# Kernel optimization log

Hardware: AMD Instinct MI355X
Metric: run time of the kernel (lower is better)

The kernel has to match this reference:

```python
import jax, jax.numpy as jnp
import numpy as np

NUM_EMBEDDINGS = 4096
EMBEDDING_DIM = 128
COMMITMENT_COST = 0.25


def setup_inputs() -> dict:
    key = jax.random.key(0)
    k_x, k_w = jax.random.split(key)
    inputs = jax.random.normal(k_x, (32, 128, 32, 32), dtype=jnp.float32)
    # xavier_uniform for Embedding weight [K, D]: bound = sqrt(6/(K+D))
    bound = float(np.sqrt(6.0 / (NUM_EMBEDDINGS + EMBEDDING_DIM)))
    weight = jax.random.uniform(k_w, (NUM_EMBEDDINGS, EMBEDDING_DIM),
                                dtype=jnp.float32, minval=-bound, maxval=bound)
    return {"inputs": inputs, "weight": weight}


def reference(inputs, weight):
    K, D = weight.shape
    # channels-first 4D input with C == embedding_dim -> NHWC
    x = jnp.transpose(inputs, (0, 2, 3, 1))  # [B, H, W, D]
    input_shape = x.shape
    flat = x.reshape(-1, D)                  # [N, D]

    x_sq = jnp.sum(flat * flat, axis=1, keepdims=True)          # [N, 1]
    w_sq = jnp.sum(weight * weight, axis=1)                     # [K]
    two_xy = 2.0 * jnp.matmul(flat, weight.T)                   # [N, K]
    distances = x_sq - two_xy + w_sq[None, :] + 1e-8

    encoding_indices = jnp.argmin(distances, axis=1)            # [N] int

    quantized = weight[encoding_indices].reshape(input_shape)   # [B, H, W, D]

    q_latent_loss = jnp.mean((quantized - x) ** 2)
    e_latent_loss = jnp.mean((jax.lax.stop_gradient(quantized) - x) ** 2)
    loss = q_latent_loss + COMMITMENT_COST * e_latent_loss
    loss = jnp.where(jnp.isnan(loss) | jnp.isinf(loss), jnp.float32(0.1), loss)

    quantized_st = x + jax.lax.stop_gradient(quantized - x)

    counts = jnp.zeros((K,), dtype=jnp.float32).at[encoding_indices].add(1.0)
    avg_probs = counts / encoding_indices.shape[0]
    perplexity = jnp.exp(-jnp.sum(avg_probs * jnp.log(avg_probs + 1e-10)))

    encodings = jax.nn.one_hot(encoding_indices, K, dtype=jnp.float32)  # [N, K]

    # input was channels-first -> restore NCHW
    quantized_st = jnp.transpose(quantized_st, (0, 3, 1, 2))
    return quantized_st, loss, perplexity, encodings, encoding_indices
```

## Files before the change

### kernel.cpp

```cpp
#include <hip/hip_runtime.h>
#include <stdint.h>
#include <math.h>

#define K_CODES 4096
#define DIM 128
#define N_FLAT 32768
#define HW 1024

#define OFF_Q    0
#define OFF_LOSS 4194304
#define OFF_PERP 4194305
#define OFF_ENC  4194306
#define OFF_IDX  138412034

#define WS_PACKED 0
#define WS_COUNTS 262144
#define WS_WSQ    278528
#define WS_XSQ    294912
#define WS_PART   425984
#define WS_XHL    430080
#define WS_WHL    (WS_XHL + 16777216)

typedef _Float16 f16x8 __attribute__((ext_vector_type(8)));
typedef float    f32x4 __attribute__((ext_vector_type(4)));


__global__ __launch_bounds__(256) void wsq_kernel(const float* __restrict__ w,
                                                  float* __restrict__ wsq,
                                                  float* __restrict__ counts) {
    int wave = threadIdx.x >> 6, lane = threadIdx.x & 63;
    int k = blockIdx.x * 4 + wave;
    float a = w[k * DIM + lane];
    float b = w[k * DIM + lane + 64];
    float s = a * a + b * b;
    #pragma unroll
    for (int o = 32; o > 0; o >>= 1) s += __shfl_down(s, o, 64);
    if (lane == 0) { wsq[k] = s; counts[k] = 0.f; }
}

__global__ __launch_bounds__(256) void wplanes_kernel(const float* __restrict__ w,
                                                      _Float16* __restrict__ whl) {
    int T = blockIdx.x * 256 + threadIdx.x;
    int k = T >> 2, seg = T & 3;
    const float* wp = w + (size_t)k * DIM + seg * 32;
    _Float16* row = whl + (size_t)k * 256;
    #pragma unroll
    for (int q = 0; q < 4; ++q) {
        float4 a = *(const float4*)(wp + q * 8);
        float4 b = *(const float4*)(wp + q * 8 + 4);
        float vv[8] = {a.x, a.y, a.z, a.w, b.x, b.y, b.z, b.w};
        f16x8 hv, lv;
        #pragma unroll
        for (int j = 0; j < 8; ++j) {
            float v = 1024.0f * vv[j];
            _Float16 h = (_Float16)v;
            _Float16 l = (_Float16)(v - (float)h);
            hv[j] = h; lv[j] = l;
        }
        *(f16x8*)(row + seg * 32 + q * 8) = hv;
        *(f16x8*)(row + 128 + seg * 32 + q * 8) = lv;
    }
}

__global__ __launch_bounds__(256) void xprep_kernel(const float* __restrict__ x,
                                                    _Float16* __restrict__ xhl,
                                                    float* __restrict__ xsq,
                                                    unsigned long long* __restrict__ packed) {
    __shared__ float xt[128 * 65];
    const int t = threadIdx.x;
    const int n0 = blockIdx.x * 64;
    const int b = n0 >> 10, hw0 = n0 & 1023;
    const float* xg = x + (size_t)b * (DIM * HW) + hw0;
    #pragma unroll
    for (int i = 0; i < 16; ++i) {
        int idx = i * 256 + t;
        int c = idx >> 5, n2 = (idx & 31) << 1;
        float2 v = *(const float2*)(xg + c * HW + n2);
        xt[c * 65 + n2] = v.x;
        xt[c * 65 + n2 + 1] = v.y;
    }
    __syncthreads();
    if (t < 64) {
        packed[n0 + t] = ~0ull;
        float s = 0.f;
        #pragma unroll
        for (int c = 0; c < DIM; ++c) {
            float v = xt[c * 65 + t];
            s = fmaf(v, v, s);
        }
        xsq[n0 + t] = s;
    }
    const int n = t >> 2, seg = t & 3;
    _Float16* row = xhl + (size_t)(n0 + n) * 256;
    #pragma unroll
    for (int q = 0; q < 4; ++q) {
        f16x8 hv, lv;
        #pragma unroll
        for (int j = 0; j < 8; ++j) {
            float v = 32.0f * xt[(seg * 32 + q * 8 + j) * 65 + n];
            _Float16 h = (_Float16)v;
            _Float16 l = (_Float16)(v - (float)h);
            hv[j] = h; lv[j] = l;
        }
        *(f16x8*)(row + seg * 32 + q * 8) = hv;
        *(f16x8*)(row + 128 + seg * 32 + q * 8) = lv;
    }
}

__global__ __launch_bounds__(256) void dist_argmin(
    const _Float16* __restrict__ xhl, const _Float16* __restrict__ whl,
    const float* __restrict__ wsq, const float* __restrict__ xsq,
    unsigned long long* __restrict__ packed, float* __restrict__ enc)
{
    __shared__ __align__(16) _Float16 xl[128 * 72];
    __shared__ __align__(16) _Float16 wl[128 * 72];
    __shared__ float xsq_s[128];
    __shared__ unsigned long long red[128];

    const int tid  = threadIdx.x;
    const int lane = tid & 63, wave = tid >> 6;
    const int lq   = lane & 15, quad = lane >> 4;
    const int wn0  = (wave >> 1) * 64, wk0 = (wave & 1) * 64;
    const int n0   = blockIdx.x * 128;
    const int kbase = blockIdx.y * 512;

    const int sr = tid >> 3, shh = (tid >> 2) & 1, sq = tid & 3;
    const int gbase = sr * 256 + shh * 128 + sq * 8;
    const int lbase = sr * 72  + shh * 32  + sq * 8;

    float* ebase = enc + (size_t)n0 * K_CODES + kbase;
    float* efill = ebase + (size_t)(tid >> 7) * K_CODES + 2 + (tid & 127) * 4;

    if (tid < 128) {
        float2 z2; z2.x = 0.f; z2.y = 0.f;
        *(float2*)(ebase + (size_t)tid * K_CODES) = z2;
        xsq_s[tid] = xsq[n0 + tid];
        red[tid] = ~0ull;
    }

    const _Float16* xbase = xhl + (size_t)n0 * 256;

    const _Float16* xr0 = xl + (wn0 + lq) * 72 + quad * 8;
    const _Float16* wr0 = wl + (wk0 + lq) * 72 + quad * 8;

    f16x8 px[4], pw[4];
    {
        const _Float16* wb = whl + (size_t)kbase * 256;
        #pragma unroll
        for (int i = 0; i < 4; ++i) {
            px[i] = *(const f16x8*)(xbase + gbase + i * 8192);
            pw[i] = *(const f16x8*)(wb    + gbase + i * 8192);
        }
        #pragma unroll
        for (int i = 0; i < 4; ++i) {
            *(f16x8*)(xl + lbase + i * 2304) = px[i];
            *(f16x8*)(wl + lbase + i * 2304) = pw[i];
        }
    }

    f32x4 acc[4][4];
    float wk[4];

    for (int s = 0; s < 16; ++s) {
        const int ks = s >> 2, c0 = s & 3;
        const int k0 = kbase + ks * 128;
        if (c0 == 0) {
            #pragma unroll
            for (int ki = 0; ki < 4; ++ki)
                wk[ki] = wsq[k0 + wk0 + ki * 16 + lq];
            #pragma unroll
            for (int i = 0; i < 4; ++i)
                #pragma unroll
                for (int j = 0; j < 4; ++j)
                    acc[i][j] = (f32x4){0.f, 0.f, 0.f, 0.f};
        }
        __syncthreads();

        f16x8 ah[4], al[4], bh[4], bl[4];
        #pragma unroll
        for (int i = 0; i < 4; ++i) {
            ah[i] = *(const f16x8*)(xr0 + i * 16 * 72);
            al[i] = *(const f16x8*)(xr0 + i * 16 * 72 + 32);
            bh[i] = *(const f16x8*)(wr0 + i * 16 * 72);
            bl[i] = *(const f16x8*)(wr0 + i * 16 * 72 + 32);
        }

        if (s < 15) {
            const int s1 = s + 1;
            const _Float16* wb =
                whl + (size_t)(kbase + (s1 >> 2) * 128) * 256;
            const int off = gbase + (s1 & 3) * 32;
            #pragma unroll
            for (int i = 0; i < 4; ++i) {
                px[i] = *(const f16x8*)(xbase + off + i * 8192);
                pw[i] = *(const f16x8*)(wb    + off + i * 8192);
            }
        }
        {
            float4 z4; z4.x = z4.y = z4.z = z4.w = 0.f;
            #pragma unroll
            for (int j = 0; j < 4; ++j)
                *(float4*)(efill + (size_t)(s * 8 + j * 2) * K_CODES) = z4;
        }

        #pragma unroll
        for (int ki = 0; ki < 4; ++ki)
            #pragma unroll
            for (int ni = 0; ni < 4; ++ni) {
                acc[ni][ki] = __builtin_amdgcn_mfma_f32_16x16x32_f16(
                    ah[ni], bh[ki], acc[ni][ki], 0, 0, 0);
                acc[ni][ki] = __builtin_amdgcn_mfma_f32_16x16x32_f16(
                    ah[ni], bl[ki], acc[ni][ki], 0, 0, 0);
                acc[ni][ki] = __builtin_amdgcn_mfma_f32_16x16x32_f16(
                    al[ni], bh[ki], acc[ni][ki], 0, 0, 0);
            }

        if (s < 15) {
            __syncthreads();
            #pragma unroll
            for (int i = 0; i < 4; ++i) {
                *(f16x8*)(xl + lbase + i * 2304) = px[i];
                *(f16x8*)(wl + lbase + i * 2304) = pw[i];
            }
        }

        if (c0 == 3) {
            #pragma unroll
            for (int ni = 0; ni < 4; ++ni) {
                #pragma unroll
                for (int rg = 0; rg < 4; ++rg) {
                    int rowl = wn0 + ni * 16 + quad * 4 + rg;
                    float xr = xsq_s[rowl];
                    float best = 3.4e38f; int bk = 0;
                    #pragma unroll
                    for (int ki = 0; ki < 4; ++ki) {
                        int kl = wk0 + ki * 16 + lq;
                        float t = xr - acc[ni][ki][rg] * 6.103515625e-05f;
                        t += wk[ki];
                        t += 1e-8f;
                        if (t < best) { best = t; bk = k0 + kl; }
                    }
                    unsigned u = __float_as_uint(best);
                    u = (u & 0x80000000u) ? ~u : (u | 0x80000000u);
                    unsigned long long p =
                        ((unsigned long long)u << 32) | (unsigned)bk;
                    #pragma unroll
                    for (int m = 1; m < 16; m <<= 1) {
                        unsigned long long o = __shfl_xor(p, m, 64);
                        if (o < p) p = o;
                    }
                    if (lq == 0) atomicMin(&red[rowl], p);
                }
            }
        }
    }

    __syncthreads();
    if (tid < 128) atomicMin(&packed[n0 + tid], red[tid]);
}

__global__ __launch_bounds__(256) void combine(
    const unsigned long long* __restrict__ packed,
    float* __restrict__ idxf, float* __restrict__ enc,
    float* __restrict__ counts)
{
    int n = blockIdx.x * 256 + threadIdx.x;
    unsigned k = (unsigned)(packed[n] & 0xFFFFFFFFu);
    idxf[n] = (float)k;
    enc[(size_t)n * K_CODES + k] = 1.0f;
    atomicAdd(&counts[k], 1.0f);
}

__global__ __launch_bounds__(256) void quantize_loss(
    const float* __restrict__ x, const float* __restrict__ w,
    const float* __restrict__ idxf, float* __restrict__ outq,
    float* __restrict__ part)
{
    const int base4 = (blockIdx.x * 256 + threadIdx.x) * 4;
    float s = 0.f;
    #pragma unroll
    for (int i = 0; i < 4; ++i) {
        int e  = base4 + i * 1048576;
        int hw = e & 1023;
        int c  = (e >> 10) & 127;
        int b  = e >> 17;
        int n  = (b << 10) | hw;
        float4 xv = *(const float4*)(x + e);
        float4 kf = *(const float4*)(idxf + n);
        float q0 = w[(int)kf.x * DIM + c];
        float q1 = w[(int)kf.y * DIM + c];
        float q2 = w[(int)kf.z * DIM + c];
        float q3 = w[(int)kf.w * DIM + c];
        float4 df; df.x = q0 - xv.x; df.y = q1 - xv.y;
                   df.z = q2 - xv.z; df.w = q3 - xv.w;
        float4 o;  o.x = xv.x + df.x; o.y = xv.y + df.y;
                   o.z = xv.z + df.z; o.w = xv.w + df.w;
        *(float4*)(outq + e) = o;
        s = fmaf(df.x, df.x, s);
        s = fmaf(df.y, df.y, s);
        s = fmaf(df.z, df.z, s);
        s = fmaf(df.w, df.w, s);
    }
    #pragma unroll
    for (int o = 32; o > 0; o >>= 1) s += __shfl_down(s, o, 64);
    __shared__ float ls[4];
    if ((threadIdx.x & 63) == 0) ls[threadIdx.x >> 6] = s;
    __syncthreads();
    if (threadIdx.x == 0) part[blockIdx.x] = ls[0] + ls[1] + ls[2] + ls[3];
}

__global__ __launch_bounds__(256) void finalize(
    const float* __restrict__ counts, const float* __restrict__ part,
    float* __restrict__ out)
{
    __shared__ float sh[512];
    float h = 0.f;
    for (int k = threadIdx.x; k < K_CODES; k += 256) {
        float p = counts[k] * (1.0f / N_FLAT);
        h += p * logf(p + 1e-10f);
    }
    float s = 0.f;
    for (int i = threadIdx.x; i < 1024; i += 256) s += part[i];
    sh[threadIdx.x] = h;
    sh[256 + threadIdx.x] = s;
    __syncthreads();
    #pragma unroll
    for (int st = 128; st > 0; st >>= 1) {
        if (threadIdx.x < st) {
            sh[threadIdx.x] += sh[threadIdx.x + st];
            sh[256 + threadIdx.x] += sh[256 + threadIdx.x + st];
        }
        __syncthreads();
    }
    if (threadIdx.x == 0) {
        float perp = expf(-sh[0]);
        float loss = 1.25f * (sh[256] / 4194304.0f);
        if (isnan(loss) || isinf(loss)) loss = 0.1f;
        out[OFF_LOSS] = loss;
        out[OFF_PERP] = perp;
    }
}

extern "C" void kernel_launch(void* const* d_in, const int* in_sizes, int n_in,
                              void* d_out, int out_size, void* d_ws, size_t ws_size,
                              hipStream_t stream) {
    const float* x = (const float*)d_in[0];
    const float* w = (const float*)d_in[1];
    float* out = (float*)d_out;
    char* ws = (char*)d_ws;

    unsigned long long* packed = (unsigned long long*)(ws + WS_PACKED);
    float* counts = (float*)(ws + WS_COUNTS);
    float* wsq    = (float*)(ws + WS_WSQ);
    float* xsq    = (float*)(ws + WS_XSQ);
    float* part   = (float*)(ws + WS_PART);
    _Float16* xhl = (_Float16*)(ws + WS_XHL);
    _Float16* whl = (_Float16*)(ws + WS_WHL);

    wsq_kernel<<<K_CODES / 4, 256, 0, stream>>>(w, wsq, counts);
    wplanes_kernel<<<K_CODES * 4 / 256, 256, 0, stream>>>(w, whl);
    xprep_kernel<<<N_FLAT / 64, 256, 0, stream>>>(x, xhl, xsq, packed);

    dim3 g2(256, 8);
    dist_argmin<<<g2, 256, 0, stream>>>(xhl, whl, wsq, xsq, packed,
                                        out + OFF_ENC);

    combine<<<N_FLAT / 256, 256, 0, stream>>>(packed, out + OFF_IDX,
                                              out + OFF_ENC, counts);

    quantize_loss<<<1024, 256, 0, stream>>>(x, w, out + OFF_IDX,
                                            out + OFF_Q, part);

    finalize<<<1, 256, 0, stream>>>(counts, part, out);
}
```

Baseline: 793.2 us.

## Double-buffer LDS tiles in dist_argmin and move one-hot zero-fill to memset

Tiles for x and codebook in shared memory are double-buffered, and global loads are prefetched two steps ahead, so each iteration needs only one barrier instead of two. The zeroing of the large one-hot encoding output is removed from the distance kernel and done by a separate hipMemsetAsync before the kernels. This cuts sync stalls in the MFMA loop but doubles LDS use, which may lower occupancy. It also gives up overlapping the zero-fill writes with compute.

```diff
diff --git a/kernel.cpp b/kernel.cpp
--- a/kernel.cpp
+++ b/kernel.cpp
@@ -110,10 +110,10 @@
 __global__ __launch_bounds__(256) void dist_argmin(
     const _Float16* __restrict__ xhl, const _Float16* __restrict__ whl,
     const float* __restrict__ wsq, const float* __restrict__ xsq,
-    unsigned long long* __restrict__ packed, float* __restrict__ enc)
+    unsigned long long* __restrict__ packed)
 {
-    __shared__ __align__(16) _Float16 xl[128 * 72];
-    __shared__ __align__(16) _Float16 wl[128 * 72];
+    __shared__ __align__(16) _Float16 xl[2][128 * 72];
+    __shared__ __align__(16) _Float16 wl[2][128 * 72];
     __shared__ float xsq_s[128];
     __shared__ unsigned long long red[128];
 
@@ -128,20 +128,15 @@
     const int gbase = sr * 256 + shh * 128 + sq * 8;
     const int lbase = sr * 72  + shh * 32  + sq * 8;
 
-    float* ebase = enc + (size_t)n0 * K_CODES + kbase;
-    float* efill = ebase + (size_t)(tid >> 7) * K_CODES + 2 + (tid & 127) * 4;
-
     if (tid < 128) {
-        float2 z2; z2.x = 0.f; z2.y = 0.f;
-        *(float2*)(ebase + (size_t)tid * K_CODES) = z2;
         xsq_s[tid] = xsq[n0 + tid];
         red[tid] = ~0ull;
     }
 
     const _Float16* xbase = xhl + (size_t)n0 * 256;
 
-    const _Float16* xr0 = xl + (wn0 + lq) * 72 + quad * 8;
-    const _Float16* wr0 = wl + (wk0 + lq) * 72 + quad * 8;
+    const int fx = (wn0 + lq) * 72 + quad * 8;
+    const int fw = (wk0 + lq) * 72 + quad * 8;
 
     f16x8 px[4], pw[4];
     {
@@ -153,8 +148,14 @@
         }
         #pragma unroll
         for (int i = 0; i < 4; ++i) {
-            *(f16x8*)(xl + lbase + i * 2304) = px[i];
-            *(f16x8*)(wl + lbase + i * 2304) = pw[i];
+            *(f16x8*)(&xl[0][lbase + i * 2304]) = px[i];
+            *(f16x8*)(&wl[0][lbase + i * 2304]) = pw[i];
+        }
+        const int off1 = gbase + 32;
+        #pragma unroll
+        for (int i = 0; i < 4; ++i) {
+            px[i] = *(const f16x8*)(xbase + off1 + i * 8192);
+            pw[i] = *(const f16x8*)(wb    + off1 + i * 8192);
         }
     }
 
@@ -162,6 +163,7 @@
     float wk[4];
 
     for (int s = 0; s < 16; ++s) {
+        const int p  = s & 1;
         const int ks = s >> 2, c0 = s & 3;
         const int k0 = kbase + ks * 128;
         if (c0 == 0) {
@@ -179,28 +181,30 @@
         f16x8 ah[4], al[4], bh[4], bl[4];
         #pragma unroll
         for (int i = 0; i < 4; ++i) {
-            ah[i] = *(const f16x8*)(xr0 + i * 16 * 72);
-            al[i] = *(const f16x8*)(xr0 + i * 16 * 72 + 32);
-            bh[i] = *(const f16x8*)(wr0 + i * 16 * 72);
-            bl[i] = *(const f16x8*)(wr0 + i * 16 * 72 + 32);
+            ah[i] = *(const f16x8*)(&xl[p][fx + i * 16 * 72]);
+            al[i] = *(const f16x8*)(&xl[p][fx + i * 16 * 72 + 32]);
+            bh[i] = *(const f16x8*)(&wl[p][fw + i * 16 * 72]);
+            bl[i] = *(const f16x8*)(&wl[p][fw + i * 16 * 72 + 32]);
         }
 
         if (s < 15) {
-            const int s1 = s + 1;
+            #pragma unroll
+            for (int i = 0; i < 4; ++i) {
+                *(f16x8*)(&xl[p ^ 1][lbase + i * 2304]) = px[i];
+                *(f16x8*)(&wl[p ^ 1][lbase + i * 2304]) = pw[i];
+            }
+        }
+
+        if (s < 14) {
+            const int s2 = s + 2;
             const _Float16* wb =
-                whl + (size_t)(kbase + (s1 >> 2) * 128) * 256;
-            const int off = gbase + (s1 & 3) * 32;
+                whl + (size_t)(kbase + (s2 >> 2) * 128) * 256;
+            const int off = gbase + (s2 & 3) * 32;
             #pragma unroll
             for (int i = 0; i < 4; ++i) {
                 px[i] = *(const f16x8*)(xbase + off + i * 8192);
                 pw[i] = *(const f16x8*)(wb    + off + i * 8192);
             }
-        }
-        {
-            float4 z4; z4.x = z4.y = z4.z = z4.w = 0.f;
-            #pragma unroll
-            for (int j = 0; j < 4; ++j)
-                *(float4*)(efill + (size_t)(s * 8 + j * 2) * K_CODES) = z4;
         }
 
         #pragma unroll
@@ -214,15 +218,6 @@
                 acc[ni][ki] = __builtin_amdgcn_mfma_f32_16x16x32_f16(
                     al[ni], bh[ki], acc[ni][ki], 0, 0, 0);
             }
-
-        if (s < 15) {
-            __syncthreads();
-            #pragma unroll
-            for (int i = 0; i < 4; ++i) {
-                *(f16x8*)(xl + lbase + i * 2304) = px[i];
-                *(f16x8*)(wl + lbase + i * 2304) = pw[i];
-            }
-        }
 
         if (c0 == 3) {
             #pragma unroll
@@ -242,14 +237,14 @@
                     }
                     unsigned u = __float_as_uint(best);
                     u = (u & 0x80000000u) ? ~u : (u | 0x80000000u);
-                    unsigned long long p =
+                    unsigned long long pck =
                         ((unsigned long long)u << 32) | (unsigned)bk;
                     #pragma unroll
                     for (int m = 1; m < 16; m <<= 1) {
-                        unsigned long long o = __shfl_xor(p, m, 64);
-                        if (o < p) p = o;
+                        unsigned long long o = __shfl_xor(pck, m, 64);
+                        if (o < pck) pck = o;
                     }
-                    if (lq == 0) atomicMin(&red[rowl], p);
+                    if (lq == 0) atomicMin(&red[rowl], pck);
                 }
             }
         }
@@ -357,13 +352,14 @@
     _Float16* xhl = (_Float16*)(ws + WS_XHL);
     _Float16* whl = (_Float16*)(ws + WS_WHL);
 
+    hipMemsetAsync(out + OFF_ENC, 0, (size_t)N_FLAT * K_CODES * 4, stream);
+
     wsq_kernel<<<K_CODES / 4, 256, 0, stream>>>(w, wsq, counts);
     wplanes_kernel<<<K_CODES * 4 / 256, 256, 0, stream>>>(w, whl);
     xprep_kernel<<<N_FLAT / 64, 256, 0, stream>>>(x, xhl, xsq, packed);
 
     dim3 g2(256, 8);
-    dist_argmin<<<g2, 256, 0, stream>>>(xhl, whl, wsq, xsq, packed,
-                                        out + OFF_ENC);
+    dist_argmin<<<g2, 256, 0, stream>>>(xhl, whl, wsq, xsq, packed);
 
     combine<<<N_FLAT / 256, 256, 0, stream>>>(packed, out + OFF_IDX,
                                               out + OFF_ENC, counts);
```

Measured after the change: 820.7 us. +3.5%, slower.

## Double-buffer LDS tiles using direct global-to-LDS loads with XOR swizzle

Applied to the files above, without the earlier changes.

Replaces the register-staged global-to-shared copy with global_load_lds direct transfers into a double-buffered LDS tile, using an XOR-swizzled layout instead of padding to avoid bank conflicts. This removes the second barrier per step and the register round-trip, so the next tile's loads can overlap with the MFMA work on the current buffer. The enc zero-fill indexing is also reorganised to coalesced rows. It doubles LDS usage, which may lower occupancy, and relies on correct ordering of async LDS writes against the single barrier.

```diff
diff --git a/kernel.cpp b/kernel.cpp
--- a/kernel.cpp
+++ b/kernel.cpp
@@ -112,8 +112,8 @@
     const float* __restrict__ wsq, const float* __restrict__ xsq,
     unsigned long long* __restrict__ packed, float* __restrict__ enc)
 {
-    __shared__ __align__(16) _Float16 xl[128 * 72];
-    __shared__ __align__(16) _Float16 wl[128 * 72];
+    __shared__ __align__(16) char xlds[2][16384];
+    __shared__ __align__(16) char wlds[2][16384];
     __shared__ float xsq_s[128];
     __shared__ unsigned long long red[128];
 
@@ -124,13 +124,18 @@
     const int n0   = blockIdx.x * 128;
     const int kbase = blockIdx.y * 512;
 
-    const int sr = tid >> 3, shh = (tid >> 2) & 1, sq = tid & 3;
-    const int gbase = sr * 256 + shh * 128 + sq * 8;
-    const int lbase = sr * 72  + shh * 32  + sq * 8;
+    const int r0 = wave * 32 + (lane >> 3);
+    const int lc = (((lane & 7) ^ (lane >> 3)) << 4);
+    const int lcAdj = lc + ((lc >> 6) * 192);
+    const char* xB = (const char*)xhl;
+    const char* wB = (const char*)whl;
+    const size_t xrow0 = (size_t)(n0 + r0) * 512;
+
+    const int swz  = (lq & 7) << 4;
+    const int hoff = (quad << 4) ^ swz;
+    const int loff = (64 | (quad << 4)) ^ swz;
 
     float* ebase = enc + (size_t)n0 * K_CODES + kbase;
-    float* efill = ebase + (size_t)(tid >> 7) * K_CODES + 2 + (tid & 127) * 4;
-
     if (tid < 128) {
         float2 z2; z2.x = 0.f; z2.y = 0.f;
         *(float2*)(ebase + (size_t)tid * K_CODES) = z2;
@@ -138,23 +143,18 @@
         red[tid] = ~0ull;
     }
 
-    const _Float16* xbase = xhl + (size_t)n0 * 256;
-
-    const _Float16* xr0 = xl + (wn0 + lq) * 72 + quad * 8;
-    const _Float16* wr0 = wl + (wk0 + lq) * 72 + quad * 8;
-
-    f16x8 px[4], pw[4];
+#define GLOAD16(gp, lp) __builtin_amdgcn_global_load_lds(                      \
+        (const __attribute__((address_space(1))) void*)(gp),                   \
+        (__attribute__((address_space(3))) void*)(lp), 16, 0, 0)
+
     {
-        const _Float16* wb = whl + (size_t)kbase * 256;
+        const size_t wrow0 = (size_t)(kbase + r0) * 512;
         #pragma unroll
         for (int i = 0; i < 4; ++i) {
-            px[i] = *(const f16x8*)(xbase + gbase + i * 8192);
-            pw[i] = *(const f16x8*)(wb    + gbase + i * 8192);
-        }
-        #pragma unroll
-        for (int i = 0; i < 4; ++i) {
-            *(f16x8*)(xl + lbase + i * 2304) = px[i];
-            *(f16x8*)(wl + lbase + i * 2304) = pw[i];
+            GLOAD16(xB + xrow0 + (size_t)i * 4096 + lcAdj,
+                    xlds[0] + wave * 4096 + i * 1024);
+            GLOAD16(wB + wrow0 + (size_t)i * 4096 + lcAdj,
+                    wlds[0] + wave * 4096 + i * 1024);
         }
     }
 
@@ -162,6 +162,7 @@
     float wk[4];
 
     for (int s = 0; s < 16; ++s) {
+        const int p  = s & 1;
         const int ks = s >> 2, c0 = s & 3;
         const int k0 = kbase + ks * 128;
         if (c0 == 0) {
@@ -177,30 +178,39 @@
         __syncthreads();
 
         f16x8 ah[4], al[4], bh[4], bl[4];
+        const char* xb = xlds[p];
+        const char* wb = wlds[p];
         #pragma unroll
         for (int i = 0; i < 4; ++i) {
-            ah[i] = *(const f16x8*)(xr0 + i * 16 * 72);
-            al[i] = *(const f16x8*)(xr0 + i * 16 * 72 + 32);
-            bh[i] = *(const f16x8*)(wr0 + i * 16 * 72);
-            bl[i] = *(const f16x8*)(wr0 + i * 16 * 72 + 32);
+            int xr = (wn0 + 16 * i + lq) * 128;
+            ah[i] = *(const f16x8*)(xb + xr + hoff);
+            al[i] = *(const f16x8*)(xb + xr + loff);
+            int wr = (wk0 + 16 * i + lq) * 128;
+            bh[i] = *(const f16x8*)(wb + wr + hoff);
+            bl[i] = *(const f16x8*)(wb + wr + loff);
         }
 
         if (s < 15) {
-            const int s1 = s + 1;
-            const _Float16* wb =
-                whl + (size_t)(kbase + (s1 >> 2) * 128) * 256;
-            const int off = gbase + (s1 & 3) * 32;
+            const int s1 = s + 1, ks1 = s1 >> 2, c01 = s1 & 3;
+            const int offX = c01 * 64 + lcAdj;
+            const size_t wrow0 = (size_t)(kbase + ks1 * 128 + r0) * 512;
+            char* xd = xlds[p ^ 1] + wave * 4096;
+            char* wd = wlds[p ^ 1] + wave * 4096;
             #pragma unroll
             for (int i = 0; i < 4; ++i) {
-                px[i] = *(const f16x8*)(xbase + off + i * 8192);
-                pw[i] = *(const f16x8*)(wb    + off + i * 8192);
+                GLOAD16(xB + xrow0 + (size_t)i * 4096 + offX, xd + i * 1024);
+                GLOAD16(wB + wrow0 + (size_t)i * 4096 + offX, wd + i * 1024);
             }
         }
+
         {
             float4 z4; z4.x = z4.y = z4.z = z4.w = 0.f;
             #pragma unroll
-            for (int j = 0; j < 4; ++j)
-                *(float4*)(efill + (size_t)(s * 8 + j * 2) * K_CODES) = z4;
+            for (int j = 0; j < 4; ++j) {
+                int idx = s * 1024 + j * 256 + tid;
+                int r = idx >> 7, c4 = idx & 127;
+                *(float4*)(ebase + (size_t)r * K_CODES + 2 + c4 * 4) = z4;
+            }
         }
 
         #pragma unroll
@@ -214,15 +224,6 @@
                 acc[ni][ki] = __builtin_amdgcn_mfma_f32_16x16x32_f16(
                     al[ni], bh[ki], acc[ni][ki], 0, 0, 0);
             }
-
-        if (s < 15) {
-            __syncthreads();
-            #pragma unroll
-            for (int i = 0; i < 4; ++i) {
-                *(f16x8*)(xl + lbase + i * 2304) = px[i];
-                *(f16x8*)(wl + lbase + i * 2304) = pw[i];
-            }
-        }
 
         if (c0 == 3) {
             #pragma unroll
@@ -242,18 +243,19 @@
                     }
                     unsigned u = __float_as_uint(best);
                     u = (u & 0x80000000u) ? ~u : (u | 0x80000000u);
-                    unsigned long long p =
+                    unsigned long long pck =
                         ((unsigned long long)u << 32) | (unsigned)bk;
                     #pragma unroll
                     for (int m = 1; m < 16; m <<= 1) {
-                        unsigned long long o = __shfl_xor(p, m, 64);
-                        if (o < p) p = o;
+                        unsigned long long o = __shfl_xor(pck, m, 64);
+                        if (o < pck) pck = o;
                     }
-                    if (lq == 0) atomicMin(&red[rowl], p);
+                    if (lq == 0) atomicMin(&red[rowl], pck);
                 }
             }
         }
     }
+#undef GLOAD16
 
     __syncthreads();
     if (tid < 128) atomicMin(&packed[n0 + tid], red[tid]);
```

After: 770.1 us. 2.9% less time.
